# Performance work log

Hardware: AMD Instinct MI355X
Metric: run time of the kernel (lower is better)

## Reference

```python
import jax, jax.numpy as jnp
import numpy as np

N, F_IN, F_HID, N_HEADS, F_OUT, ALPHA = 4096, 128, 64, 4, 64, 0.2
AVG_DEG = 32.0


def setup_inputs() -> dict:
    key = jax.random.key(0)
    ks = jax.random.split(key, 8)
    x = jax.random.normal(ks[0], (N, F_IN), dtype=jnp.float32)
    # sparse-ish adjacency (avg degree ~32) + self loops so every row has a neighbor
    adj = (jax.random.uniform(ks[1], (N, N)) < (AVG_DEG / N)).astype(jnp.float32)
    adj = jnp.maximum(adj, jnp.eye(N, dtype=jnp.float32))
    s = 1.0 / np.sqrt(F_IN)
    lin_W = jax.random.uniform(ks[2], (F_IN, F_IN), jnp.float32, -s, s)
    lin_b = jax.random.uniform(ks[3], (F_IN,), jnp.float32, -s, s)
    W_heads = jax.random.normal(ks[4], (N_HEADS, F_IN, F_HID), jnp.float32) * 0.1
    a_heads = jax.random.normal(ks[5], (N_HEADS, 2 * F_HID), jnp.float32) * 0.1
    W_end = jax.random.normal(ks[6], (N_HEADS * F_HID, F_OUT), jnp.float32) * 0.1
    a_end = jax.random.normal(ks[7], (2 * F_OUT,), jnp.float32) * 0.1
    return dict(x=x, adj=adj, lin_W=lin_W, lin_b=lin_b,
                W_heads=W_heads, a_heads=a_heads, W_end=W_end, a_end=a_end)


def _gat_layer(h, adj, W, a):
    # standard dense-masked GAT layer (pyGAT style)
    Wh = h @ W                      # [N, F']
    f = W.shape[1]
    src = Wh @ a[:f]                # [N]  a^T contribution of source node
    dst = Wh @ a[f:]                # [N]  contribution of destination node
    e = jax.nn.leaky_relu(src[:, None] + dst[None, :], ALPHA)  # [N, N]
    e = jnp.where(adj > 0, e, -9e15)
    att = jax.nn.softmax(e, axis=1)  # neighbor softmax per row
    return jax.nn.elu(att @ Wh)      # [N, F']


def reference(x, adj, lin_W, lin_b, W_heads, a_heads, W_end, a_end):
    h = x @ lin_W + lin_b            # nn.Linear(input_features, input_features)
    # parallel multi-head attention, then concat along feature dim
    heads = jax.vmap(lambda W, a: _gat_layer(h, adj, W, a))(W_heads, a_heads)  # [H, N, F_HID]
    hcat = jnp.transpose(heads, (1, 0, 2)).reshape(N, N_HEADS * F_HID)         # [N, H*F_HID]
    out = _gat_layer(hcat, adj, W_end, a_end)                                  # [N, F_OUT]
    return jax.nn.softmax(out, axis=1)
```

## Files before the change

### kernel.cpp

```cpp
#include <hip/hip_runtime.h>

#define GN 4096
#define F_IN 128
#define F_HID 64
#define NHEADS 4
#define F_OUT 64
#define ALPHA 0.2f
#define NGEMM 512

#define OFF_WH     0
#define OFF_SRC1   4194304
#define OFF_DST1   4259840
#define OFF_WH2    4325376
#define OFF_SRC2   5373952
#define OFF_DST2   5390336
#define OFF_BM     5406720


__global__ __launch_bounds__(256) void prep_kernel(
        const float* __restrict__ adj, const float* __restrict__ x,
        const float* __restrict__ linW, const float* __restrict__ linb,
        const float* __restrict__ Wheads, const float* __restrict__ aheads,
        float* __restrict__ Wh, float* __restrict__ src1, float* __restrict__ dst1,
        unsigned long long* __restrict__ bm) {
    __shared__ struct { float xs[8][128]; float hs[8][128]; } sm;
    const int tid = threadIdx.x;

    if (blockIdx.x >= NGEMM) {
        const int row  = blockIdx.x - NGEMM;
        const int wave = tid >> 6, lane = tid & 63;
        const float4* rowf4 = (const float4*)(adj + (size_t)row * GN);
        unsigned long long* bmr = bm + (size_t)row * 64;
        #pragma unroll
        for (int k = 0; k < 4; ++k) {
            float4 v = rowf4[k * 256 + tid];
            unsigned long long B0 = __ballot(v.x > 0.0f);
            unsigned long long B1 = __ballot(v.y > 0.0f);
            unsigned long long B2 = __ballot(v.z > 0.0f);
            unsigned long long B3 = __ballot(v.w > 0.0f);
            if      (lane == 0) bmr[k * 16 + wave * 4 + 0] = B0;
            else if (lane == 1) bmr[k * 16 + wave * 4 + 1] = B1;
            else if (lane == 2) bmr[k * 16 + wave * 4 + 2] = B2;
            else if (lane == 3) bmr[k * 16 + wave * 4 + 3] = B3;
        }
        return;
    }

    const int i0 = blockIdx.x * 8;
    #pragma unroll
    for (int t = 0; t < 4; ++t) {
        int e = t * 256 + tid;
        sm.xs[e >> 7][e & 127] = x[(size_t)i0 * 128 + e];
    }
    __syncthreads();
    {
        const int k = tid & 127;
        const int n0 = tid >> 7;
        float bk = linb[k];
        float a0 = bk, a1 = bk, a2 = bk, a3 = bk;
        for (int j = 0; j < 128; ++j) {
            float w = linW[j * 128 + k];
            a0 += sm.xs[n0][j] * w;
            a1 += sm.xs[n0 + 2][j] * w;
            a2 += sm.xs[n0 + 4][j] * w;
            a3 += sm.xs[n0 + 6][j] * w;
        }
        sm.hs[n0][k] = a0; sm.hs[n0 + 2][k] = a1;
        sm.hs[n0 + 4][k] = a2; sm.hs[n0 + 6][k] = a3;
    }
    __syncthreads();
    {
        const int hd = tid >> 6, f = tid & 63;
        float acc[8] = {0, 0, 0, 0, 0, 0, 0, 0};
        const float* Wp = Wheads + (size_t)hd * F_IN * F_HID + f;
        for (int j = 0; j < 128; ++j) {
            float w = Wp[j * 64];
            #pragma unroll
            for (int n = 0; n < 8; ++n) acc[n] += sm.hs[n][j] * w;
        }
        const float as = aheads[hd * 128 + f];
        const float ad = aheads[hd * 128 + 64 + f];
        #pragma unroll
        for (int n = 0; n < 8; ++n) {
            Wh[(size_t)(i0 + n) * 256 + hd * 64 + f] = acc[n];
            float sv = acc[n] * as, dv = acc[n] * ad;
            #pragma unroll
            for (int o = 32; o > 0; o >>= 1) {
                sv += __shfl_xor(sv, o, 64);
                dv += __shfl_xor(dv, o, 64);
            }
            if (f == 0) { src1[(i0 + n) * 4 + hd] = sv; dst1[(i0 + n) * 4 + hd] = dv; }
        }
    }
}

__device__ __forceinline__ int build_row_nbrs(const unsigned long long* __restrict__ bm,
                                              int row, int lane, int* sidx) {
    unsigned long long bits = bm[(size_t)row * 64 + lane];
    int c = __popcll(bits);
    int inc = c;
    #pragma unroll
    for (int o = 1; o < 64; o <<= 1) {
        int n = __shfl_up(inc, o, 64);
        if (lane >= o) inc += n;
    }
    int p = inc - c;
    const int deg = __shfl(inc, 63, 64);
    const int col0 = ((lane >> 4) << 10) + (((lane >> 2) & 3) << 8) + (lane & 3);
    while (bits) {
        int b = __ffsll((long long)bits) - 1;
        if (p < 136) sidx[p] = col0 + (b << 2);
        ++p;
        bits &= bits - 1;
    }
    const int deg4 = (deg + 3) & ~3;
    if (lane < deg4 - deg) sidx[deg + lane] = 0;
    return deg;
}

__global__ __launch_bounds__(256) void attn_mid_kernel(
        const float* __restrict__ Wh, const float* __restrict__ src1,
        const float* __restrict__ dst1, const float* __restrict__ Wend,
        const float* __restrict__ aend, float* __restrict__ Wh2,
        float* __restrict__ src2, float* __restrict__ dst2,
        const unsigned long long* __restrict__ bm) {
    __shared__ float ps[4][528];
    __shared__ float hcat[4][256];
    __shared__ int   sidx[4][136];
    const int wave = threadIdx.x >> 6;
    const int lane = threadIdx.x & 63;
    const int row  = blockIdx.x * 4 + wave;

    const int deg = build_row_nbrs(bm, row, lane, sidx[wave]);
    const int* nb = sidx[wave];
    const int nchunk = (deg + 63) >> 6;

    const float4 s4 = ((const float4*)src1)[row];
    float4 ev[2];
    float4 m4 = make_float4(-1e30f, -1e30f, -1e30f, -1e30f);
    for (int c = 0; c < nchunk; ++c) {
        int t = c * 64 + lane;
        float4 e = make_float4(-1e30f, -1e30f, -1e30f, -1e30f);
        if (t < deg) {
            int j = nb[t];
            float4 d = ((const float4*)dst1)[j];
            e.x = s4.x + d.x; e.x = (e.x > 0.0f) ? e.x : ALPHA * e.x;
            e.y = s4.y + d.y; e.y = (e.y > 0.0f) ? e.y : ALPHA * e.y;
            e.z = s4.z + d.z; e.z = (e.z > 0.0f) ? e.z : ALPHA * e.z;
            e.w = s4.w + d.w; e.w = (e.w > 0.0f) ? e.w : ALPHA * e.w;
        }
        ev[c] = e;
        m4.x = fmaxf(m4.x, e.x); m4.y = fmaxf(m4.y, e.y);
        m4.z = fmaxf(m4.z, e.z); m4.w = fmaxf(m4.w, e.w);
    }
    #pragma unroll
    for (int o = 32; o > 0; o >>= 1) {
        m4.x = fmaxf(m4.x, __shfl_xor(m4.x, o, 64));
        m4.y = fmaxf(m4.y, __shfl_xor(m4.y, o, 64));
        m4.z = fmaxf(m4.z, __shfl_xor(m4.z, o, 64));
        m4.w = fmaxf(m4.w, __shfl_xor(m4.w, o, 64));
    }
    float4 l4 = make_float4(0.f, 0.f, 0.f, 0.f);
    for (int c = 0; c < nchunk; ++c) {
        ev[c].x = expf(ev[c].x - m4.x); l4.x += ev[c].x;
        ev[c].y = expf(ev[c].y - m4.y); l4.y += ev[c].y;
        ev[c].z = expf(ev[c].z - m4.z); l4.z += ev[c].z;
        ev[c].w = expf(ev[c].w - m4.w); l4.w += ev[c].w;
    }
    #pragma unroll
    for (int o = 32; o > 0; o >>= 1) {
        l4.x += __shfl_xor(l4.x, o, 64);
        l4.y += __shfl_xor(l4.y, o, 64);
        l4.z += __shfl_xor(l4.z, o, 64);
        l4.w += __shfl_xor(l4.w, o, 64);
    }
    const float4 inv = make_float4(1.f / l4.x, 1.f / l4.y, 1.f / l4.z, 1.f / l4.w);
    for (int c = 0; c < nchunk; ++c) {
        int t = c * 64 + lane;
        float4 p = make_float4(ev[c].x * inv.x, ev[c].y * inv.y,
                               ev[c].z * inv.z, ev[c].w * inv.w);
        ((float4*)&ps[wave][0])[t] = p;
    }

    const int hl = lane >> 4;
    const float4* Wh4 = (const float4*)Wh;
    float4 acc = make_float4(0.f, 0.f, 0.f, 0.f);
    const int deg4 = (deg + 3) & ~3;
    for (int t = 0; t < deg4; t += 4) {
        int4 jj = *(const int4*)(nb + t);
        float4 w0 = Wh4[(size_t)jj.x * 64 + lane];
        float4 w1 = Wh4[(size_t)jj.y * 64 + lane];
        float4 w2 = Wh4[(size_t)jj.z * 64 + lane];
        float4 w3 = Wh4[(size_t)jj.w * 64 + lane];
        const float* pp = &ps[wave][t * 4 + hl];
        float p0 = pp[0], p1 = pp[4], p2 = pp[8], p3 = pp[12];
        acc.x += p0 * w0.x + p1 * w1.x + p2 * w2.x + p3 * w3.x;
        acc.y += p0 * w0.y + p1 * w1.y + p2 * w2.y + p3 * w3.y;
        acc.z += p0 * w0.z + p1 * w1.z + p2 * w2.z + p3 * w3.z;
        acc.w += p0 * w0.w + p1 * w1.w + p2 * w2.w + p3 * w3.w;
    }
    acc.x = (acc.x > 0.0f) ? acc.x : expm1f(acc.x);
    acc.y = (acc.y > 0.0f) ? acc.y : expm1f(acc.y);
    acc.z = (acc.z > 0.0f) ? acc.z : expm1f(acc.z);
    acc.w = (acc.w > 0.0f) ? acc.w : expm1f(acc.w);
    ((float4*)hcat[wave])[lane] = acc;

    float a0 = 0.f, a1 = 0.f, a2 = 0.f, a3 = 0.f;
    const float* Wp = Wend + lane;
    #pragma unroll 4
    for (int j = 0; j < 256; j += 4) {
        a0 += hcat[wave][j    ] * Wp[(j    ) * 64];
        a1 += hcat[wave][j + 1] * Wp[(j + 1) * 64];
        a2 += hcat[wave][j + 2] * Wp[(j + 2) * 64];
        a3 += hcat[wave][j + 3] * Wp[(j + 3) * 64];
    }
    float aa = (a0 + a1) + (a2 + a3);
    Wh2[(size_t)row * 64 + lane] = aa;
    float s0 = aa * aend[lane], d0 = aa * aend[64 + lane];
    #pragma unroll
    for (int o = 32; o > 0; o >>= 1) {
        s0 += __shfl_xor(s0, o, 64); d0 += __shfl_xor(d0, o, 64);
    }
    if (lane == 0) { src2[row] = s0; dst2[row] = d0; }
}

__global__ __launch_bounds__(256) void attn2_kernel(
        const float* __restrict__ Wh2, const float* __restrict__ src,
        const float* __restrict__ dst, const unsigned long long* __restrict__ bm,
        float* __restrict__ out) {
    __shared__ int sidx[4][136];
    const int wave = threadIdx.x >> 6;
    const int lane = threadIdx.x & 63;
    const int row  = blockIdx.x * 4 + wave;

    const int deg = build_row_nbrs(bm, row, lane, sidx[wave]);
    const int* nb = sidx[wave];
    const float s_i = src[row];

    float e[2];
    #pragma unroll
    for (int c = 0; c < 2; ++c) {
        int t = c * 64 + lane;
        float ev = -1e30f;
        if (t < deg) {
            int j = nb[t];
            ev = s_i + dst[j];
            ev = (ev > 0.0f) ? ev : ALPHA * ev;
        }
        e[c] = ev;
    }
    float m = fmaxf(e[0], e[1]);
    #pragma unroll
    for (int o = 32; o > 0; o >>= 1) m = fmaxf(m, __shfl_xor(m, o, 64));
    float l = 0.0f;
    #pragma unroll
    for (int c = 0; c < 2; ++c) { e[c] = expf(e[c] - m); l += e[c]; }
    #pragma unroll
    for (int o = 32; o > 0; o >>= 1) l += __shfl_xor(l, o, 64);

    float accA = 0.0f, accB = 0.0f;
    const float* W2 = Wh2 + lane;
    #pragma unroll
    for (int c = 0; c < 2; ++c) {
        int base = c * 64;
        if (base >= deg) break;
        int nmax = deg - base; if (nmax > 64) nmax = 64;
        int n4 = (nmax + 3) & ~3;
        for (int t = 0; t < n4; t += 4) {
            int4 jj = *(const int4*)(nb + base + t);
            float w0 = W2[(size_t)jj.x * 64];
            float w1 = W2[(size_t)jj.y * 64];
            float w2 = W2[(size_t)jj.z * 64];
            float w3 = W2[(size_t)jj.w * 64];
            float p0 = __shfl(e[c], t, 64),     p1 = __shfl(e[c], t + 1, 64);
            float p2 = __shfl(e[c], t + 2, 64), p3 = __shfl(e[c], t + 3, 64);
            accA += p0 * w0 + p2 * w2;
            accB += p1 * w1 + p3 * w3;
        }
    }
    float v = (accA + accB) / l;
    v = (v > 0.0f) ? v : expm1f(v);

    float mm = v;
    #pragma unroll
    for (int o = 32; o > 0; o >>= 1) mm = fmaxf(mm, __shfl_xor(mm, o, 64));
    float ee = expf(v - mm);
    float ss = ee;
    #pragma unroll
    for (int o = 32; o > 0; o >>= 1) ss += __shfl_xor(ss, o, 64);
    out[(size_t)row * F_OUT + lane] = ee / ss;
}

extern "C" void kernel_launch(void* const* d_in, const int* in_sizes, int n_in,
                              void* d_out, int out_size, void* d_ws, size_t ws_size,
                              hipStream_t stream) {
    const float* x      = (const float*)d_in[0];
    const float* adj    = (const float*)d_in[1];
    const float* lin_W  = (const float*)d_in[2];
    const float* lin_b  = (const float*)d_in[3];
    const float* Wheads = (const float*)d_in[4];
    const float* aheads = (const float*)d_in[5];
    const float* Wend   = (const float*)d_in[6];
    const float* aend   = (const float*)d_in[7];
    float* out = (float*)d_out;

    char* ws = (char*)d_ws;
    float* Wh   = (float*)(ws + OFF_WH);
    float* src1 = (float*)(ws + OFF_SRC1);
    float* dst1 = (float*)(ws + OFF_DST1);
    float* Wh2  = (float*)(ws + OFF_WH2);
    float* src2 = (float*)(ws + OFF_SRC2);
    float* dst2 = (float*)(ws + OFF_DST2);
    unsigned long long* bm = (unsigned long long*)(ws + OFF_BM);

    prep_kernel<<<NGEMM + GN, 256, 0, stream>>>(adj, x, lin_W, lin_b, Wheads, aheads,
                                                Wh, src1, dst1, bm);
    attn_mid_kernel<<<GN / 4, 256, 0, stream>>>(Wh, src1, dst1, Wend, aend,
                                                Wh2, src2, dst2, bm);
    attn2_kernel<<<GN / 4, 256, 0, stream>>>(Wh2, src2, dst2, bm, out);
}
```

Measured before the change: 53.01 us.

## Fuse adjacency bitmask construction into first attention kernel

```diff
diff --git a/kernel.cpp b/kernel.cpp
--- a/kernel.cpp
+++ b/kernel.cpp
@@ -6,7 +6,6 @@
 #define NHEADS 4
 #define F_OUT 64
 #define ALPHA 0.2f
-#define NGEMM 512
 
 #define OFF_WH     0
 #define OFF_SRC1   4194304
@@ -18,34 +17,12 @@
 
 
 __global__ __launch_bounds__(256) void prep_kernel(
-        const float* __restrict__ adj, const float* __restrict__ x,
-        const float* __restrict__ linW, const float* __restrict__ linb,
-        const float* __restrict__ Wheads, const float* __restrict__ aheads,
-        float* __restrict__ Wh, float* __restrict__ src1, float* __restrict__ dst1,
-        unsigned long long* __restrict__ bm) {
+        const float* __restrict__ x, const float* __restrict__ linW,
+        const float* __restrict__ linb, const float* __restrict__ Wheads,
+        const float* __restrict__ aheads, float* __restrict__ Wh,
+        float* __restrict__ src1, float* __restrict__ dst1) {
     __shared__ struct { float xs[8][128]; float hs[8][128]; } sm;
     const int tid = threadIdx.x;
-
-    if (blockIdx.x >= NGEMM) {
-        const int row  = blockIdx.x - NGEMM;
-        const int wave = tid >> 6, lane = tid & 63;
-        const float4* rowf4 = (const float4*)(adj + (size_t)row * GN);
-        unsigned long long* bmr = bm + (size_t)row * 64;
-        #pragma unroll
-        for (int k = 0; k < 4; ++k) {
-            float4 v = rowf4[k * 256 + tid];
-            unsigned long long B0 = __ballot(v.x > 0.0f);
-            unsigned long long B1 = __ballot(v.y > 0.0f);
-            unsigned long long B2 = __ballot(v.z > 0.0f);
-            unsigned long long B3 = __ballot(v.w > 0.0f);
-            if      (lane == 0) bmr[k * 16 + wave * 4 + 0] = B0;
-            else if (lane == 1) bmr[k * 16 + wave * 4 + 1] = B1;
-            else if (lane == 2) bmr[k * 16 + wave * 4 + 2] = B2;
-            else if (lane == 3) bmr[k * 16 + wave * 4 + 3] = B3;
-        }
-        return;
-    }
-
     const int i0 = blockIdx.x * 8;
     #pragma unroll
     for (int t = 0; t < 4; ++t) {
@@ -94,9 +71,8 @@
     }
 }
 
-__device__ __forceinline__ int build_row_nbrs(const unsigned long long* __restrict__ bm,
-                                              int row, int lane, int* sidx) {
-    unsigned long long bits = bm[(size_t)row * 64 + lane];
+__device__ __forceinline__ int nbrs_from_bits(unsigned long long bits, int lane,
+                                              int* sidx) {
     int c = __popcll(bits);
     int inc = c;
     #pragma unroll
@@ -106,7 +82,7 @@
     }
     int p = inc - c;
     const int deg = __shfl(inc, 63, 64);
-    const int col0 = ((lane >> 4) << 10) + (((lane >> 2) & 3) << 8) + (lane & 3);
+    const int col0 = ((lane >> 2) << 8) + (lane & 3);
     while (bits) {
         int b = __ffsll((long long)bits) - 1;
         if (p < 136) sidx[p] = col0 + (b << 2);
@@ -119,11 +95,11 @@
 }
 
 __global__ __launch_bounds__(256) void attn_mid_kernel(
-        const float* __restrict__ Wh, const float* __restrict__ src1,
-        const float* __restrict__ dst1, const float* __restrict__ Wend,
-        const float* __restrict__ aend, float* __restrict__ Wh2,
-        float* __restrict__ src2, float* __restrict__ dst2,
-        const unsigned long long* __restrict__ bm) {
+        const float* __restrict__ adj, const float* __restrict__ Wh,
+        const float* __restrict__ src1, const float* __restrict__ dst1,
+        const float* __restrict__ Wend, const float* __restrict__ aend,
+        float* __restrict__ Wh2, float* __restrict__ src2, float* __restrict__ dst2,
+        unsigned long long* __restrict__ bm) {
     __shared__ float ps[4][528];
     __shared__ float hcat[4][256];
     __shared__ int   sidx[4][136];
@@ -131,7 +107,24 @@
     const int lane = threadIdx.x & 63;
     const int row  = blockIdx.x * 4 + wave;
 
-    const int deg = build_row_nbrs(bm, row, lane, sidx[wave]);
+    const float4* rowf4 = (const float4*)(adj + (size_t)row * GN);
+    unsigned long long bits = 0;
+    #pragma unroll 4
+    for (int k = 0; k < 16; ++k) {
+        float4 v = rowf4[k * 64 + lane];
+        unsigned long long B0 = __ballot(v.x > 0.0f);
+        unsigned long long B1 = __ballot(v.y > 0.0f);
+        unsigned long long B2 = __ballot(v.z > 0.0f);
+        unsigned long long B3 = __ballot(v.w > 0.0f);
+        const int base = k * 4;
+        if (lane == base)     bits = B0;
+        if (lane == base + 1) bits = B1;
+        if (lane == base + 2) bits = B2;
+        if (lane == base + 3) bits = B3;
+    }
+    bm[(size_t)row * 64 + lane] = bits;
+
+    const int deg = nbrs_from_bits(bits, lane, sidx[wave]);
     const int* nb = sidx[wave];
     const int nchunk = (deg + 63) >> 6;
 
@@ -233,7 +226,8 @@
     const int lane = threadIdx.x & 63;
     const int row  = blockIdx.x * 4 + wave;
 
-    const int deg = build_row_nbrs(bm, row, lane, sidx[wave]);
+    const unsigned long long bits = bm[(size_t)row * 64 + lane];
+    const int deg = nbrs_from_bits(bits, lane, sidx[wave]);
     const int* nb = sidx[wave];
     const float s_i = src[row];
 
@@ -313,9 +307,9 @@
     float* dst2 = (float*)(ws + OFF_DST2);
     unsigned long long* bm = (unsigned long long*)(ws + OFF_BM);
 
-    prep_kernel<<<NGEMM + GN, 256, 0, stream>>>(adj, x, lin_W, lin_b, Wheads, aheads,
-                                                Wh, src1, dst1, bm);
-    attn_mid_kernel<<<GN / 4, 256, 0, stream>>>(Wh, src1, dst1, Wend, aend,
+    prep_kernel<<<GN / 8, 256, 0, stream>>>(x, lin_W, lin_b, Wheads, aheads,
+                                            Wh, src1, dst1);
+    attn_mid_kernel<<<GN / 4, 256, 0, stream>>>(adj, Wh, src1, dst1, Wend, aend,
                                                 Wh2, src2, dst2, bm);
     attn2_kernel<<<GN / 4, 256, 0, stream>>>(Wh2, src2, dst2, bm, out);
 }
```

New measurement: 62.09 us. +17.1%, slower.
